# Performance work log

Measured on AMD Instinct MI355X. Metric: run time of the kernel, lower is better.

Reference implementation:

```python
import jax, jax.numpy as jnp
import numpy as np

N, E = 30000, 180000
IN, H, OUT = 3000, 512, 30


def _segment_softmax(e, dst, n):
    # numerically stable softmax over incoming edges of each destination node
    m = jax.ops.segment_max(e, dst, num_segments=n)
    m = jnp.where(jnp.isfinite(m), m, 0.0)  # nodes with no in-edges
    ex = jnp.exp(e - m[dst])
    den = jax.ops.segment_sum(ex, dst, num_segments=n)
    return ex / den[dst]


def _gat(x, src, dst, Ws, Wd, a_s, a_d, n, alpha=None):
    """edGATConv (heads=1, no self-loops, no bias).
    xs = lin_s(x); attention score from lin_s(x)[src] and lin_d(x)[dst];
    out[i] = sum_{e: dst_e=i} alpha_e * xs[src_e].
    If alpha is given (tie_alpha), reuse it instead of recomputing."""
    xs = x @ Ws.T  # [n, F_out]
    if alpha is None:
        xd = x @ Wd.T
        e = jax.nn.leaky_relu(xs[src] @ a_s + xd[dst] @ a_d, 0.2)  # [E]
        alpha = _segment_softmax(e, dst, n)
    out = jax.ops.segment_sum(alpha[:, None] * xs[src], dst, num_segments=n)
    return out, alpha


def setup_inputs() -> dict:
    key = jax.random.key(0)
    ks = jax.random.split(key, 7)
    features = jax.random.normal(ks[0], (N, IN), dtype=jnp.float32)
    edge_index = jax.random.randint(ks[1], (2, E), 0, N)
    W1s = jax.random.normal(ks[2], (H, IN), dtype=jnp.float32) * 0.02
    W1d = jax.random.normal(ks[3], (H, IN), dtype=jnp.float32) * 0.02
    a1s = jax.random.normal(ks[4], (H,), dtype=jnp.float32) * 0.1
    a1d = jax.random.normal(ks[5], (H,), dtype=jnp.float32) * 0.1
    W2s = jax.random.normal(ks[6], (OUT, H), dtype=jnp.float32) * 0.05
    return {"features": features, "edge_index": edge_index,
            "W1s": W1s, "W1d": W1d, "a1s": a1s, "a1d": a1d, "W2s": W2s}


def reference(features, edge_index, W1s, W1d, a1s, a1d, W2s):
    src, dst = edge_index[0], edge_index[1]
    n = features.shape[0]
    # conv1: attentive GAT layer, stores tie_alpha
    h1, alpha1 = _gat(features, src, dst, W1s, W1d, a1s, a1d, n)
    h1 = jax.nn.elu(h1)
    # conv2: aslinear=True -> plain linear with lin_s
    h2 = h1 @ W2s.T  # [N, OUT]
    # conv3: weights tied to conv2 transposed, alpha tied to conv1
    # W3s = W2s.T so xs3 = h2 @ W3s.T = h2 @ W2s
    h3, _ = _gat(h2, src, dst, W2s.T, None, None, None, n, alpha=alpha1)
    h3 = jax.nn.elu(h3)
    # conv4: aslinear, weight tied to conv1 transposed: h3 @ W4s.T = h3 @ W1s
    h4 = h3 @ W1s  # [N, IN]
    return (h2, h4)
```

## Files before the change

kernel.cpp:

```cpp
#include <hip/hip_runtime.h>

typedef unsigned short u16;
typedef __bf16 bf16_t;
typedef bf16_t bf16x8 __attribute__((ext_vector_type(8)));
typedef float f32x4 __attribute__((ext_vector_type(4)));
typedef u16 u16x8 __attribute__((ext_vector_type(8)));

#define AS1 __attribute__((address_space(1)))
#define AS3 __attribute__((address_space(3)))

__device__ __forceinline__ u16 f2bf(float f) {
    union { float f; unsigned u; } v; v.f = f;
    unsigned r = v.u + 0x7FFFu + ((v.u >> 16) & 1u);
    return (u16)(r >> 16);
}
__device__ __forceinline__ float bf2f(u16 s) {
    union { unsigned u; float f; } v; v.u = ((unsigned)s) << 16;
    return v.f;
}

__device__ __forceinline__ void gload_lds16(const u16* g, u16* l) {
    __builtin_amdgcn_global_load_lds((AS1 const void*)g, (AS3 void*)l, 16, 0, 0);
}

template <bool OUT_BF16, bool GUARD>
__global__ __launch_bounds__(256) void gemm_bt(
    const u16* __restrict__ A, const u16* __restrict__ B, void* __restrict__ Cv,
    int K, int ldc, int Mreal, int Nreal)
{
    __shared__ u16 As[128 * 64];
    __shared__ u16 Bs[128 * 64];
    const int t = threadIdx.x;
    const int w = t >> 6, l = t & 63;

    const int nwg = gridDim.x * gridDim.y;
    const int lin = blockIdx.y * gridDim.x + blockIdx.x;
    const int xcd = lin & 7, loc = lin >> 3;
    const int q = nwg >> 3, r = nwg & 7;
    const int swz = (xcd < r ? xcd * (q + 1) : r * (q + 1) + (xcd - r) * q) + loc;
    const int bx = swz % gridDim.x, by = swz / gridDim.x;

    const int m0 = by * 128, n0 = bx * 128;
    const int wm = (w >> 1) * 64, wn = (w & 1) * 64;

    const int srow = w << 5;
    const int lrow = l >> 3, lc = l & 7;

    f32x4 acc[4][4] = {};

    for (int kt = 0; kt < K; kt += 64) {
#pragma unroll
        for (int i = 0; i < 4; ++i) {
            int row = srow + i * 8 + lrow;
            int gc = ((lc ^ (row & 7)) << 3);
            const u16* ga = A + (size_t)(m0 + row) * K + kt + gc;
            const u16* gb = B + (size_t)(n0 + row) * K + kt + gc;
            u16* la = &As[(srow + i * 8) * 64];
            u16* lb = &Bs[(srow + i * 8) * 64];
            gload_lds16(ga, la);
            gload_lds16(gb, lb);
        }
        asm volatile("s_waitcnt vmcnt(0)");
        __syncthreads();

#pragma unroll
        for (int kk = 0; kk < 2; ++kk) {
            bf16x8 af[4], bfr[4];
            int kc = kk * 4 + (l >> 4);
#pragma unroll
            for (int mi = 0; mi < 4; ++mi) {
                int row = wm + mi * 16 + (l & 15);
                af[mi] = *(const bf16x8*)&As[row * 64 + ((kc ^ (row & 7)) << 3)];
            }
#pragma unroll
            for (int ni = 0; ni < 4; ++ni) {
                int col = wn + ni * 16 + (l & 15);
                bfr[ni] = *(const bf16x8*)&Bs[col * 64 + ((kc ^ (col & 7)) << 3)];
            }
#pragma unroll
            for (int mi = 0; mi < 4; ++mi)
#pragma unroll
                for (int ni = 0; ni < 4; ++ni)
                    acc[mi][ni] = __builtin_amdgcn_mfma_f32_16x16x32_bf16(
                        af[mi], bfr[ni], acc[mi][ni], 0, 0, 0);
        }
        __syncthreads();
    }

#pragma unroll
    for (int mi = 0; mi < 4; ++mi) {
#pragma unroll
        for (int qq = 0; qq < 4; ++qq) {
            int row = m0 + wm + mi * 16 + (l >> 4) * 4 + qq;
            if (GUARD && row >= Mreal) continue;
#pragma unroll
            for (int ni = 0; ni < 4; ++ni) {
                int col = n0 + wn + ni * 16 + (l & 15);
                if (GUARD && col >= Nreal) continue;
                float v = acc[mi][ni][qq];
                if (OUT_BF16) ((u16*)Cv)[(size_t)row * ldc + col] = f2bf(v);
                else          ((float*)Cv)[(size_t)row * ldc + col] = v;
            }
        }
    }
}

__global__ void k_vd(const float* __restrict__ W1d, const float* __restrict__ a1d,
                     float* __restrict__ vd) {
    int i = blockIdx.x * 256 + threadIdx.x;
    if (i >= 3000) return;
    float acc = 0.f;
    for (int h = 0; h < 512; ++h) acc += W1d[(size_t)h * 3000 + i] * a1d[h];
    vd[i] = acc;
}

__global__ void k_w1sb(const float* __restrict__ W1s, u16* __restrict__ wb) {
    int idx = blockIdx.x * 256 + threadIdx.x;
    if (idx >= 512 * 768) return;
    int n = idx / 768, g = idx % 768, k = g * 4;
    ushort4 o = make_ushort4(0, 0, 0, 0);
    if (k < 3000) {
        float4 v = *(const float4*)(W1s + (size_t)n * 3000 + k);
        o.x = f2bf(v.x); o.y = f2bf(v.y); o.z = f2bf(v.z); o.w = f2bf(v.w);
    }
    *(ushort4*)(wb + (size_t)n * 3072 + k) = o;
}

__global__ void k_w1st(const float* __restrict__ W1s, u16* __restrict__ wt) {
    int idx = blockIdx.x * 256 + threadIdx.x;
    if (idx >= 3072 * 512) return;
    int n = idx >> 9, k = idx & 511;
    wt[idx] = (n < 3000) ? f2bf(W1s[(size_t)k * 3000 + n]) : (u16)0;
}

__global__ void k_w2b(const float* __restrict__ W2s, u16* __restrict__ wb) {
    int idx = blockIdx.x * 256 + threadIdx.x;
    if (idx >= 128 * 512) return;
    int n = idx >> 9, k = idx & 511;
    wb[idx] = (n < 30) ? f2bf(W2s[(size_t)n * 512 + k]) : (u16)0;
}

__global__ void k_convX(const float* __restrict__ X, u16* __restrict__ xb,
                        const float* __restrict__ vd, float* __restrict__ sd) {
    __shared__ float red[4];
    int n = blockIdx.x, t = threadIdx.x;
    u16* brow = xb + (size_t)n * 3072;
    if (n < 30000) {
        const float* xrow = X + (size_t)n * 3000;
        float part = 0.f;
#pragma unroll
        for (int it = 0; it < 3; ++it) {
            int c = (t + it * 256) * 4;
            ushort4 o = make_ushort4(0, 0, 0, 0);
            if (c < 3000) {
                float4 v = *(const float4*)(xrow + c);
                float4 wv = *(const float4*)(vd + c);
                o.x = f2bf(v.x); o.y = f2bf(v.y); o.z = f2bf(v.z); o.w = f2bf(v.w);
                part += v.x * wv.x + v.y * wv.y + v.z * wv.z + v.w * wv.w;
            }
            *(ushort4*)(brow + c) = o;
        }
#pragma unroll
        for (int s = 32; s; s >>= 1) part += __shfl_xor(part, s);
        if ((t & 63) == 0) red[t >> 6] = part;
        __syncthreads();
        if (t == 0) sd[n] = red[0] + red[1] + red[2] + red[3];
    } else {
#pragma unroll
        for (int it = 0; it < 3; ++it)
            *(ushort4*)(brow + (t + it * 256) * 4) = make_ushort4(0, 0, 0, 0);
    }
}

__global__ void k_ss(const u16* __restrict__ xs1, const float* __restrict__ a1s,
                     float* __restrict__ ss) {
    int w = threadIdx.x >> 6, l = threadIdx.x & 63;
    int n = blockIdx.x * 4 + w;
    if (n >= 30000) return;
    const u16* row = xs1 + (size_t)n * 512 + l * 8;
    const float* a = a1s + l * 8;
    ushort4 u0 = *(const ushort4*)row;
    ushort4 u1 = *(const ushort4*)(row + 4);
    float4 w0 = *(const float4*)a;
    float4 w1 = *(const float4*)(a + 4);
    float acc = bf2f(u0.x) * w0.x + bf2f(u0.y) * w0.y + bf2f(u0.z) * w0.z + bf2f(u0.w) * w0.w
              + bf2f(u1.x) * w1.x + bf2f(u1.y) * w1.y + bf2f(u1.z) * w1.z + bf2f(u1.w) * w1.w;
#pragma unroll
    for (int s = 32; s; s >>= 1) acc += __shfl_xor(acc, s);
    if (l == 0) ss[n] = acc;
}

__global__ void k_deg(const int* __restrict__ dst, unsigned* __restrict__ deg) {
    int j = blockIdx.x * 256 + threadIdx.x;
    if (j < 180000) atomicAdd(&deg[dst[j]], 1u);
}

__global__ void k_scan1(const unsigned* __restrict__ deg, unsigned* __restrict__ bsum, int n) {
    __shared__ unsigned ws[4];
    int i = blockIdx.x * 256 + threadIdx.x;
    unsigned v = (i < n) ? deg[i] : 0u;
#pragma unroll
    for (int s = 32; s; s >>= 1) v += __shfl_xor(v, s);
    if ((threadIdx.x & 63) == 0) ws[threadIdx.x >> 6] = v;
    __syncthreads();
    if (threadIdx.x == 0) bsum[blockIdx.x] = ws[0] + ws[1] + ws[2] + ws[3];
}

__global__ void k_scan2(const unsigned* __restrict__ bsum, unsigned* __restrict__ boff,
                        unsigned* __restrict__ off_end, int nb) {
    __shared__ unsigned tmp[128];
    int t = threadIdx.x;
    unsigned v = (t < nb) ? bsum[t] : 0u;
    tmp[t] = v;
    __syncthreads();
    for (int s = 1; s < 128; s <<= 1) {
        unsigned a = (t >= s) ? tmp[t - s] : 0u;
        __syncthreads();
        tmp[t] += a;
        __syncthreads();
    }
    if (t < nb) boff[t] = tmp[t] - v;
    if (t == nb - 1) *off_end = tmp[t];
}

__global__ void k_scan3(const unsigned* __restrict__ deg, const unsigned* __restrict__ boff,
                        unsigned* __restrict__ off, unsigned* __restrict__ cur, int n) {
    __shared__ unsigned tmp[256];
    int b = blockIdx.x, t = threadIdx.x, i = b * 256 + t;
    unsigned v = (i < n) ? deg[i] : 0u;
    tmp[t] = v;
    __syncthreads();
    for (int s = 1; s < 256; s <<= 1) {
        unsigned a = (t >= s) ? tmp[t - s] : 0u;
        __syncthreads();
        tmp[t] += a;
        __syncthreads();
    }
    if (i < n) {
        unsigned o = boff[b] + tmp[t] - v;
        off[i] = o;
        cur[i] = o;
    }
}

__global__ void k_fill(const int* __restrict__ dst, unsigned* __restrict__ cur,
                       unsigned* __restrict__ csr) {
    int j = blockIdx.x * 256 + threadIdx.x;
    if (j >= 180000) return;
    unsigned pos = atomicAdd(&cur[dst[j]], 1u);
    csr[pos] = (unsigned)j;
}

__global__ void k_soft(const int* __restrict__ src, const float* __restrict__ ss,
                       const float* __restrict__ sd, float* __restrict__ alpha,
                       const unsigned* __restrict__ csr, const unsigned* __restrict__ off) {
    int t = threadIdx.x;
    int g = t >> 3, l = t & 7;
    int n = blockIdx.x * 32 + g;
    if (n >= 30000) return;
    unsigned lo = off[n], hi = off[n + 1];
    if (lo == hi) return;
    float sdn = sd[n];
    float m = -1e30f;
    for (unsigned i = lo + l; i < hi; i += 8) {
        float v = ss[src[csr[i]]] + sdn;
        v = v > 0.f ? v : 0.2f * v;
        m = fmaxf(m, v);
    }
    m = fmaxf(m, __shfl_xor(m, 1));
    m = fmaxf(m, __shfl_xor(m, 2));
    m = fmaxf(m, __shfl_xor(m, 4));
    float den = 0.f;
    for (unsigned i = lo + l; i < hi; i += 8) {
        float v = ss[src[csr[i]]] + sdn;
        v = v > 0.f ? v : 0.2f * v;
        den += expf(v - m);
    }
    den += __shfl_xor(den, 1);
    den += __shfl_xor(den, 2);
    den += __shfl_xor(den, 4);
    float inv = 1.f / den;
    for (unsigned i = lo + l; i < hi; i += 8) {
        unsigned j = csr[i];
        float v = ss[src[j]] + sdn;
        v = v > 0.f ? v : 0.2f * v;
        alpha[j] = expf(v - m) * inv;
    }
}

__global__ void k_agg(const u16* __restrict__ xin, const float* __restrict__ alpha,
                      const unsigned* __restrict__ csr, const unsigned* __restrict__ off,
                      const int* __restrict__ src, u16* __restrict__ outb, int nvalid) {
    int w = threadIdx.x >> 6, l = threadIdx.x & 63;
    int n = blockIdx.x * 4 + w;
    float acc[8] = {};
    if (n < nvalid) {
        unsigned lo = off[n], hi = off[n + 1];
        for (unsigned i = lo; i < hi; ++i) {
            unsigned j = csr[i];
            float av = alpha[j];
            int sj = src[j];
            u16x8 row = *(const u16x8*)&xin[(size_t)sj * 512 + l * 8];
#pragma unroll
            for (int k = 0; k < 8; ++k) acc[k] += av * bf2f(row[k]);
        }
    }
    u16x8 o;
#pragma unroll
    for (int k = 0; k < 8; ++k) {
        float a = acc[k] > 0.f ? acc[k] : expf(acc[k]) - 1.f;
        o[k] = f2bf(a);
    }
    *(u16x8*)&outb[(size_t)n * 512 + l * 8] = o;
}

__global__ void k_xs3(const float* __restrict__ h2, const float* __restrict__ W2s,
                      u16* __restrict__ xs3) {
    int t = threadIdx.x;
    size_t n0 = (size_t)blockIdx.x * 8;
    float w0[30], w1[30];
#pragma unroll
    for (int o = 0; o < 30; ++o) {
        w0[o] = W2s[(size_t)o * 512 + t];
        w1[o] = W2s[(size_t)o * 512 + t + 256];
    }
    for (int r = 0; r < 8; ++r) {
        size_t n = n0 + r;
        const float* hr = h2 + n * 30;
        float a0 = 0.f, a1 = 0.f;
#pragma unroll
        for (int o = 0; o < 30; ++o) {
            float v = hr[o];
            a0 += v * w0[o];
            a1 += v * w1[o];
        }
        xs3[n * 512 + t] = f2bf(a0);
        xs3[n * 512 + t + 256] = f2bf(a1);
    }
}

extern "C" void kernel_launch(void* const* d_in, const int* in_sizes, int n_in,
                              void* d_out, int out_size, void* d_ws, size_t ws_size,
                              hipStream_t stream) {
    const float* X   = (const float*)d_in[0];
    const int*   ei  = (const int*)d_in[1];
    const float* W1s = (const float*)d_in[2];
    const float* W1d = (const float*)d_in[3];
    const float* a1s = (const float*)d_in[4];
    const float* a1d = (const float*)d_in[5];
    const float* W2s = (const float*)d_in[6];
    const int* src = ei;
    const int* dst = ei + 180000;

    float* out = (float*)d_out;
    float* h2 = out;
    float* h4 = out + 900000;

    char* ob = (char*)(out + 900000);
    u16* xbf  = (u16*)ob;
    u16* xs1b = (u16*)(ob + 184811520);
    u16* h1b  = (u16*)(ob + 184811520 + 30801920);
    u16* xs3b = (u16*)(ob + 184811520 + 30801920 + 30801920);

    char* w = (char*)d_ws;
    auto carve = [&](size_t bytes) { char* p = w; w += (bytes + 255) & ~(size_t)255; return p; };
    u16* w1sb = (u16*)carve((size_t)512 * 3072 * 2);
    u16* w1st = (u16*)carve((size_t)3072 * 512 * 2);
    u16* w2sb = (u16*)carve((size_t)128 * 512 * 2);
    u16* h3b  = (u16*)carve((size_t)30080 * 512 * 2);
    float* vd    = (float*)carve(3000 * 4);
    float* ss    = (float*)carve(30000 * 4);
    float* sd    = (float*)carve(30000 * 4);
    float* alpha = (float*)carve(180000 * 4);
    unsigned* deg = (unsigned*)carve(30000 * 4);
    unsigned* off = (unsigned*)carve(30004 * 4);
    unsigned* cur = (unsigned*)carve(30000 * 4);
    unsigned* csr = (unsigned*)carve(180000 * 4);
    unsigned* bsum = (unsigned*)carve(128 * 4);
    unsigned* boff = (unsigned*)carve(128 * 4);

    hipMemsetAsync(deg, 0, 30000 * 4, stream);

    k_vd  <<<12, 256, 0, stream>>>(W1d, a1d, vd);
    k_w1sb<<<1536, 256, 0, stream>>>(W1s, w1sb);
    k_w1st<<<6144, 256, 0, stream>>>(W1s, w1st);
    k_w2b <<<256, 256, 0, stream>>>(W2s, w2sb);
    k_convX<<<30080, 256, 0, stream>>>(X, xbf, vd, sd);

    gemm_bt<true, false><<<dim3(4, 235), 256, 0, stream>>>(xbf, w1sb, xs1b, 3072, 512, 0, 0);

    k_ss  <<<7500, 256, 0, stream>>>(xs1b, a1s, ss);
    k_deg <<<704, 256, 0, stream>>>(dst, deg);
    k_scan1<<<118, 256, 0, stream>>>(deg, bsum, 30000);
    k_scan2<<<1, 128, 0, stream>>>(bsum, boff, &off[30000], 118);
    k_scan3<<<118, 256, 0, stream>>>(deg, boff, off, cur, 30000);
    k_fill<<<704, 256, 0, stream>>>(dst, cur, csr);
    k_soft<<<938, 256, 0, stream>>>(src, ss, sd, alpha, csr, off);

    k_agg <<<7520, 256, 0, stream>>>(xs1b, alpha, csr, off, src, h1b, 30000);

    gemm_bt<false, true><<<dim3(1, 235), 256, 0, stream>>>(h1b, w2sb, h2, 512, 30, 30000, 30);

    k_xs3 <<<3750, 256, 0, stream>>>(h2, W2s, xs3b);
    k_agg <<<7520, 256, 0, stream>>>(xs3b, alpha, csr, off, src, h3b, 30000);

    gemm_bt<false, true><<<dim3(24, 235), 256, 0, stream>>>(h3b, w1st, h4, 512, 3000, 30000, 3000);
}
```

Measured before the change: 711.5 us.

## Fuse prep kernels, fold source score into input pass, trim K padding

Measured after the change: 681.5 us. -4.2%, faster.

```diff
diff --git a/kernel.cpp b/kernel.cpp
--- a/kernel.cpp
+++ b/kernel.cpp
@@ -105,94 +105,102 @@
     }
 }
 
-__global__ void k_vd(const float* __restrict__ W1d, const float* __restrict__ a1d,
-                     float* __restrict__ vd) {
-    int i = blockIdx.x * 256 + threadIdx.x;
-    if (i >= 3000) return;
-    float acc = 0.f;
-    for (int h = 0; h < 512; ++h) acc += W1d[(size_t)h * 3000 + i] * a1d[h];
-    vd[i] = acc;
-}
-
-__global__ void k_w1sb(const float* __restrict__ W1s, u16* __restrict__ wb) {
-    int idx = blockIdx.x * 256 + threadIdx.x;
-    if (idx >= 512 * 768) return;
-    int n = idx / 768, g = idx % 768, k = g * 4;
-    ushort4 o = make_ushort4(0, 0, 0, 0);
-    if (k < 3000) {
-        float4 v = *(const float4*)(W1s + (size_t)n * 3000 + k);
-        o.x = f2bf(v.x); o.y = f2bf(v.y); o.z = f2bf(v.z); o.w = f2bf(v.w);
-    }
-    *(ushort4*)(wb + (size_t)n * 3072 + k) = o;
-}
-
-__global__ void k_w1st(const float* __restrict__ W1s, u16* __restrict__ wt) {
-    int idx = blockIdx.x * 256 + threadIdx.x;
-    if (idx >= 3072 * 512) return;
-    int n = idx >> 9, k = idx & 511;
-    wt[idx] = (n < 3000) ? f2bf(W1s[(size_t)k * 3000 + n]) : (u16)0;
-}
-
-__global__ void k_w2b(const float* __restrict__ W2s, u16* __restrict__ wb) {
-    int idx = blockIdx.x * 256 + threadIdx.x;
-    if (idx >= 128 * 512) return;
-    int n = idx >> 9, k = idx & 511;
-    wb[idx] = (n < 30) ? f2bf(W2s[(size_t)n * 512 + k]) : (u16)0;
+__global__ void k_prep(const float* __restrict__ W1d, const float* __restrict__ a1d,
+                       const float* __restrict__ W1s, const float* __restrict__ a1s,
+                       const float* __restrict__ W2s, const int* __restrict__ dst,
+                       float* __restrict__ vd, float* __restrict__ vs,
+                       u16* __restrict__ w1sb, u16* __restrict__ w1st,
+                       u16* __restrict__ w2sb, unsigned* __restrict__ deg) {
+    int b = blockIdx.x, t = threadIdx.x;
+    if (b < 12) {
+        int i = b * 256 + t;
+        if (i >= 3000) return;
+        float ad = 0.f, as = 0.f;
+        for (int h = 0; h < 512; ++h) {
+            ad += W1d[(size_t)h * 3000 + i] * a1d[h];
+            as += W1s[(size_t)h * 3000 + i] * a1s[h];
+        }
+        vd[i] = ad;
+        vs[i] = as;
+    } else if (b < 1516) {
+        int idx = (b - 12) * 256 + t;
+        int n = idx / 752, k = (idx % 752) * 4;
+        ushort4 o = make_ushort4(0, 0, 0, 0);
+        if (k < 3000) {
+            float4 v = *(const float4*)(W1s + (size_t)n * 3000 + k);
+            o.x = f2bf(v.x); o.y = f2bf(v.y); o.z = f2bf(v.z); o.w = f2bf(v.w);
+        }
+        *(ushort4*)(w1sb + (size_t)n * 3008 + k) = o;
+    } else if (b < 1900) {
+        __shared__ float tile[64][65];
+        int fb = b - 1516;
+        int i0 = (fb % 48) * 64, h0 = (fb / 48) * 64;
+        int il = t & 63, hq = t >> 6;
+#pragma unroll
+        for (int rr = 0; rr < 16; ++rr) {
+            int hl = rr * 4 + hq;
+            int i = i0 + il;
+            tile[hl][il] = (i < 3000) ? W1s[(size_t)(h0 + hl) * 3000 + i] : 0.f;
+        }
+        __syncthreads();
+#pragma unroll
+        for (int rr = 0; rr < 16; ++rr) {
+            int il2 = rr * 4 + hq;
+            w1st[(size_t)(i0 + il2) * 512 + h0 + il] = f2bf(tile[il][il2]);
+        }
+    } else if (b < 2156) {
+        int idx = (b - 1900) * 256 + t;
+        int n = idx >> 9, k = idx & 511;
+        w2sb[idx] = (n < 30) ? f2bf(W2s[(size_t)n * 512 + k]) : (u16)0;
+    } else {
+        int j = (b - 2156) * 256 + t;
+        if (j < 180000) atomicAdd(&deg[dst[j]], 1u);
+    }
 }
 
 __global__ void k_convX(const float* __restrict__ X, u16* __restrict__ xb,
-                        const float* __restrict__ vd, float* __restrict__ sd) {
-    __shared__ float red[4];
+                        const float* __restrict__ vd, const float* __restrict__ vs,
+                        float* __restrict__ sd, float* __restrict__ ss) {
+    __shared__ float redd[4], reds[4];
     int n = blockIdx.x, t = threadIdx.x;
-    u16* brow = xb + (size_t)n * 3072;
+    u16* brow = xb + (size_t)n * 3008;
     if (n < 30000) {
         const float* xrow = X + (size_t)n * 3000;
-        float part = 0.f;
+        float pd = 0.f, ps = 0.f;
 #pragma unroll
         for (int it = 0; it < 3; ++it) {
             int c = (t + it * 256) * 4;
-            ushort4 o = make_ushort4(0, 0, 0, 0);
             if (c < 3000) {
                 float4 v = *(const float4*)(xrow + c);
-                float4 wv = *(const float4*)(vd + c);
+                float4 wd = *(const float4*)(vd + c);
+                float4 wvs = *(const float4*)(vs + c);
+                ushort4 o;
                 o.x = f2bf(v.x); o.y = f2bf(v.y); o.z = f2bf(v.z); o.w = f2bf(v.w);
-                part += v.x * wv.x + v.y * wv.y + v.z * wv.z + v.w * wv.w;
+                pd += v.x * wd.x + v.y * wd.y + v.z * wd.z + v.w * wd.w;
+                ps += v.x * wvs.x + v.y * wvs.y + v.z * wvs.z + v.w * wvs.w;
+                *(ushort4*)(brow + c) = o;
+            } else if (c < 3008) {
+                *(ushort4*)(brow + c) = make_ushort4(0, 0, 0, 0);
             }
-            *(ushort4*)(brow + c) = o;
-        }
-#pragma unroll
-        for (int s = 32; s; s >>= 1) part += __shfl_xor(part, s);
-        if ((t & 63) == 0) red[t >> 6] = part;
-        __syncthreads();
-        if (t == 0) sd[n] = red[0] + red[1] + red[2] + red[3];
+        }
+#pragma unroll
+        for (int s = 32; s; s >>= 1) {
+            pd += __shfl_xor(pd, s);
+            ps += __shfl_xor(ps, s);
+        }
+        if ((t & 63) == 0) { redd[t >> 6] = pd; reds[t >> 6] = ps; }
+        __syncthreads();
+        if (t == 0) {
+            sd[n] = redd[0] + redd[1] + redd[2] + redd[3];
+            ss[n] = reds[0] + reds[1] + reds[2] + reds[3];
+        }
     } else {
 #pragma unroll
-        for (int it = 0; it < 3; ++it)
-            *(ushort4*)(brow + (t + it * 256) * 4) = make_ushort4(0, 0, 0, 0);
-    }
-}
-
-__global__ void k_ss(const u16* __restrict__ xs1, const float* __restrict__ a1s,
-                     float* __restrict__ ss) {
-    int w = threadIdx.x >> 6, l = threadIdx.x & 63;
-    int n = blockIdx.x * 4 + w;
-    if (n >= 30000) return;
-    const u16* row = xs1 + (size_t)n * 512 + l * 8;
-    const float* a = a1s + l * 8;
-    ushort4 u0 = *(const ushort4*)row;
-    ushort4 u1 = *(const ushort4*)(row + 4);
-    float4 w0 = *(const float4*)a;
-    float4 w1 = *(const float4*)(a + 4);
-    float acc = bf2f(u0.x) * w0.x + bf2f(u0.y) * w0.y + bf2f(u0.z) * w0.z + bf2f(u0.w) * w0.w
-              + bf2f(u1.x) * w1.x + bf2f(u1.y) * w1.y + bf2f(u1.z) * w1.z + bf2f(u1.w) * w1.w;
-#pragma unroll
-    for (int s = 32; s; s >>= 1) acc += __shfl_xor(acc, s);
-    if (l == 0) ss[n] = acc;
-}
-
-__global__ void k_deg(const int* __restrict__ dst, unsigned* __restrict__ deg) {
-    int j = blockIdx.x * 256 + threadIdx.x;
-    if (j < 180000) atomicAdd(&deg[dst[j]], 1u);
+        for (int it = 0; it < 3; ++it) {
+            int c = (t + it * 256) * 4;
+            if (c < 3008) *(ushort4*)(brow + c) = make_ushort4(0, 0, 0, 0);
+        }
+    }
 }
 
 __global__ void k_scan1(const unsigned* __restrict__ deg, unsigned* __restrict__ bsum, int n) {
@@ -206,27 +214,27 @@
     if (threadIdx.x == 0) bsum[blockIdx.x] = ws[0] + ws[1] + ws[2] + ws[3];
 }
 
-__global__ void k_scan2(const unsigned* __restrict__ bsum, unsigned* __restrict__ boff,
-                        unsigned* __restrict__ off_end, int nb) {
-    __shared__ unsigned tmp[128];
-    int t = threadIdx.x;
-    unsigned v = (t < nb) ? bsum[t] : 0u;
-    tmp[t] = v;
+__global__ void k_scanB(const unsigned* __restrict__ deg, const unsigned* __restrict__ bsum,
+                        unsigned* __restrict__ off, unsigned* __restrict__ cur,
+                        int n, int nb) {
+    __shared__ unsigned tmp[256];
+    __shared__ unsigned bo;
+    int b = blockIdx.x, t = threadIdx.x, i = b * 256 + t;
+    if (t < 64) {
+        unsigned s0 = (t < nb) ? bsum[t] : 0u;
+        unsigned s1 = (t + 64 < nb) ? bsum[t + 64] : 0u;
+        unsigned v = ((t < b) ? s0 : 0u) + ((t + 64 < b) ? s1 : 0u);
+#pragma unroll
+        for (int s = 32; s; s >>= 1) v += __shfl_xor(v, s);
+        if (t == 0) bo = v;
+        if (b == nb - 1) {
+            unsigned tv = s0 + s1;
+#pragma unroll
+            for (int s = 32; s; s >>= 1) tv += __shfl_xor(tv, s);
+            if (t == 0) off[n] = tv;
+        }
+    }
     __syncthreads();
-    for (int s = 1; s < 128; s <<= 1) {
-        unsigned a = (t >= s) ? tmp[t - s] : 0u;
-        __syncthreads();
-        tmp[t] += a;
-        __syncthreads();
-    }
-    if (t < nb) boff[t] = tmp[t] - v;
-    if (t == nb - 1) *off_end = tmp[t];
-}
-
-__global__ void k_scan3(const unsigned* __restrict__ deg, const unsigned* __restrict__ boff,
-                        unsigned* __restrict__ off, unsigned* __restrict__ cur, int n) {
-    __shared__ unsigned tmp[256];
-    int b = blockIdx.x, t = threadIdx.x, i = b * 256 + t;
     unsigned v = (i < n) ? deg[i] : 0u;
     tmp[t] = v;
     __syncthreads();
@@ -237,7 +245,7 @@
         __syncthreads();
     }
     if (i < n) {
-        unsigned o = boff[b] + tmp[t] - v;
+        unsigned o = bo + tmp[t] - v;
         off[i] = o;
         cur[i] = o;
     }
@@ -296,13 +304,23 @@
     float acc[8] = {};
     if (n < nvalid) {
         unsigned lo = off[n], hi = off[n + 1];
-        for (unsigned i = lo; i < hi; ++i) {
-            unsigned j = csr[i];
-            float av = alpha[j];
-            int sj = src[j];
-            u16x8 row = *(const u16x8*)&xin[(size_t)sj * 512 + l * 8];
-#pragma unroll
-            for (int k = 0; k < 8; ++k) acc[k] += av * bf2f(row[k]);
+        unsigned i = lo;
+        for (; i + 2 <= hi; i += 2) {
+            unsigned j0 = csr[i], j1 = csr[i + 1];
+            float a0 = alpha[j0], a1 = alpha[j1];
+            int s0 = src[j0], s1 = src[j1];
+            u16x8 r0 = *(const u16x8*)&xin[(size_t)s0 * 512 + l * 8];
+            u16x8 r1 = *(const u16x8*)&xin[(size_t)s1 * 512 + l * 8];
+#pragma unroll
+            for (int k = 0; k < 8; ++k) acc[k] += a0 * bf2f(r0[k]) + a1 * bf2f(r1[k]);
+        }
+        if (i < hi) {
+            unsigned j0 = csr[i];
+            float a0 = alpha[j0];
+            int s0 = src[j0];
+            u16x8 r0 = *(const u16x8*)&xin[(size_t)s0 * 512 + l * 8];
+#pragma unroll
+            for (int k = 0; k < 8; ++k) acc[k] += a0 * bf2f(r0[k]);
         }
     }
     u16x8 o;
@@ -358,17 +376,18 @@
 
     char* ob = (char*)(out + 900000);
     u16* xbf  = (u16*)ob;
-    u16* xs1b = (u16*)(ob + 184811520);
-    u16* h1b  = (u16*)(ob + 184811520 + 30801920);
-    u16* xs3b = (u16*)(ob + 184811520 + 30801920 + 30801920);
+    u16* xs1b = (u16*)(ob + 180961280);
+    u16* h1b  = (u16*)(ob + 180961280 + 30801920);
+    u16* xs3b = (u16*)(ob + 180961280 + 30801920 + 30801920);
 
     char* w = (char*)d_ws;
     auto carve = [&](size_t bytes) { char* p = w; w += (bytes + 255) & ~(size_t)255; return p; };
-    u16* w1sb = (u16*)carve((size_t)512 * 3072 * 2);
-    u16* w1st = (u16*)carve((size_t)3072 * 512 * 2);
-    u16* w2sb = (u16*)carve((size_t)128 * 512 * 2);
-    u16* h3b  = (u16*)carve((size_t)30080 * 512 * 2);
-    float* vd    = (float*)carve(3000 * 4);
+    u16* w1sb  = (u16*)carve((size_t)512 * 3008 * 2);
+    u16* w1st  = (u16*)carve((size_t)3072 * 512 * 2);
+    u16* w2sb  = (u16*)carve((size_t)128 * 512 * 2);
+    u16* h3b   = (u16*)carve((size_t)30080 * 512 * 2);
+    float* vd    = (float*)carve(3008 * 4);
+    float* vs    = (float*)carve(3008 * 4);
     float* ss    = (float*)carve(30000 * 4);
     float* sd    = (float*)carve(30000 * 4);
     float* alpha = (float*)carve(180000 * 4);
@@ -377,23 +396,18 @@
     unsigned* cur = (unsigned*)carve(30000 * 4);
     unsigned* csr = (unsigned*)carve(180000 * 4);
     unsigned* bsum = (unsigned*)carve(128 * 4);
-    unsigned* boff = (unsigned*)carve(128 * 4);
 
     hipMemsetAsync(deg, 0, 30000 * 4, stream);
 
-    k_vd  <<<12, 256, 0, stream>>>(W1d, a1d, vd);
-    k_w1sb<<<1536, 256, 0, stream>>>(W1s, w1sb);
-    k_w1st<<<6144, 256, 0, stream>>>(W1s, w1st);
-    k_w2b <<<256, 256, 0, stream>>>(W2s, w2sb);
-    k_convX<<<30080, 256, 0, stream>>>(X, xbf, vd, sd);
-
-    gemm_bt<true, false><<<dim3(4, 235), 256, 0, stream>>>(xbf, w1sb, xs1b, 3072, 512, 0, 0);
-
-    k_ss  <<<7500, 256, 0, stream>>>(xs1b, a1s, ss);
-    k_deg <<<704, 256, 0, stream>>>(dst, deg);
+    k_prep<<<2860, 256, 0, stream>>>(W1d, a1d, W1s, a1s, W2s, dst,
+                                     vd, vs, w1sb, w1st, w2sb, deg);
+
+    k_convX<<<30080, 256, 0, stream>>>(X, xbf, vd, vs, sd, ss);
+
+    gemm_bt<true, false><<<dim3(4, 235), 256, 0, stream>>>(xbf, w1sb, xs1b, 3008, 512, 0, 0);
+
     k_scan1<<<118, 256, 0, stream>>>(deg, bsum, 30000);
-    k_scan2<<<1, 128, 0, stream>>>(bsum, boff, &off[30000], 118);
-    k_scan3<<<118, 256, 0, stream>>>(deg, boff, off, cur, 30000);
+    k_scanB<<<118, 256, 0, stream>>>(deg, bsum, off, cur, 30000, 118);
     k_fill<<<704, 256, 0, stream>>>(dst, cur, csr);
     k_soft<<<938, 256, 0, stream>>>(src, ss, sd, alpha, csr, off);
 
```
